# Kernel tuning notes

Hardware: AMD Instinct MI355X
Metric: run time of the kernel (lower is better)

Reference implementation:

```python
import jax, jax.numpy as jnp
import numpy as np

N_NODES = 100000
N_EDGES = 1600000
IN_CH = 128
OUT_CH = 64
HID = 2 * OUT_CH


def setup_inputs() -> dict:
    key = jax.random.key(0)
    ks = jax.random.split(key, 9)
    x = jax.random.normal(ks[0], (N_NODES, IN_CH), dtype=jnp.float32)
    edge_index = jax.random.randint(ks[1], (2, N_EDGES), 0, N_NODES, dtype=jnp.int64)
    s = 0.05
    W1 = jax.random.normal(ks[2], (IN_CH, HID), dtype=jnp.float32) * s
    b1 = jnp.zeros((HID,), dtype=jnp.float32)
    Wmu = jax.random.normal(ks[3], (HID, OUT_CH), dtype=jnp.float32) * s
    bmu = jnp.zeros((OUT_CH,), dtype=jnp.float32)
    Wls = jax.random.normal(ks[4], (HID, OUT_CH), dtype=jnp.float32) * s
    bls = jnp.zeros((OUT_CH,), dtype=jnp.float32)
    eps = jax.random.normal(ks[5], (N_NODES, OUT_CH), dtype=jnp.float32)
    return {"x": x, "edge_index": edge_index, "W1": W1, "b1": b1,
            "Wmu": Wmu, "bmu": bmu, "Wls": Wls, "bls": bls, "eps": eps}


def _gcn_conv(x, W, b, src, dst, dis):
    # PyG GCNConv: out = D^{-1/2}(A+I)D^{-1/2} X W + b, self-loops added.
    h = x @ W  # [N, F]
    norm = dis[src] * dis[dst]  # per-edge symmetric norm
    msg = h[src] * norm[:, None]  # [E, F] gathered + scaled messages
    agg = jax.ops.segment_sum(msg, dst, num_segments=x.shape[0])
    agg = agg + h * (dis * dis)[:, None]  # self-loop term
    return agg + b


def reference(x, edge_index, W1, b1, Wmu, bmu, Wls, bls, eps):
    src, dst = edge_index[0], edge_index[1]
    N = x.shape[0]
    # degree over A + I (aggregation at dst, +1 for self loop)
    deg = jax.ops.segment_sum(jnp.ones_like(dst, dtype=x.dtype), dst,
                              num_segments=N) + 1.0
    dis = jax.lax.rsqrt(deg)  # deg >= 1, safe
    h = _gcn_conv(x, W1, b1, src, dst, dis)
    mu = _gcn_conv(h, Wmu, bmu, src, dst, dis)
    logstd = _gcn_conv(h, Wls, bls, src, dst, dis)
    z = mu + eps * jnp.exp(logstd)  # reparametrization trick
    return (z, mu, logstd)
```

## Files before the change

kernel.cpp:

```cpp
#include <hip/hip_runtime.h>
#include <hip/hip_bf16.h>


typedef unsigned int u32;
typedef unsigned short u16;
typedef unsigned char u8;
typedef __bf16 bf16x8 __attribute__((ext_vector_type(8)));
typedef float f32x4 __attribute__((ext_vector_type(4)));
typedef int i32x4 __attribute__((ext_vector_type(4)));

__device__ __forceinline__ u16 f2bf(float f) {
    union { float f; u32 u; } v; v.f = f;
    u32 u = v.u;
    u += 0x7fffu + ((u >> 16) & 1u);
    return (u16)(u >> 16);
}
__device__ __forceinline__ float bflo(u32 p) {
    union { u32 u; float f; } v; v.u = p << 16; return v.f;
}
__device__ __forceinline__ float bfhi(u32 p) {
    union { u32 u; float f; } v; v.u = p & 0xffff0000u; return v.f;
}

__global__ __launch_bounds__(256) void deg_hist(const int* __restrict__ dst,
                                                u32* __restrict__ deg,
                                                u8* __restrict__ loc, int E) {
    int i4 = (blockIdx.x * 256 + threadIdx.x) * 4;
    if (i4 + 3 < E) {
        i32x4 d4 = __builtin_nontemporal_load((const i32x4*)(dst + i4));
        u32 l0 = atomicAdd(&deg[d4.x], 1u) & 0xffu;
        u32 l1 = atomicAdd(&deg[d4.y], 1u) & 0xffu;
        u32 l2 = atomicAdd(&deg[d4.z], 1u) & 0xffu;
        u32 l3 = atomicAdd(&deg[d4.w], 1u) & 0xffu;
        u32 packed = l0 | (l1 << 8) | (l2 << 16) | (l3 << 24);
        __builtin_nontemporal_store(packed, (u32*)(loc + i4));
    } else {
        for (int i = i4; i < E; ++i) loc[i] = (u8)atomicAdd(&deg[dst[i]], 1u);
    }
}

__global__ __launch_bounds__(256) void scanA(const u32* __restrict__ deg,
                                             u32* __restrict__ blockSums, int N) {
    __shared__ u32 s[256];
    int t = threadIdx.x, i = blockIdx.x * 256 + t;
    s[t] = (i < N) ? deg[i] : 0u;
    for (int off = 128; off > 0; off >>= 1) {
        __syncthreads();
        if (t < off) s[t] += s[t + off];
    }
    if (t == 0) blockSums[blockIdx.x] = s[0];
}

__global__ __launch_bounds__(512) void scanB(const u32* __restrict__ blockSums,
                                             u32* __restrict__ blockOffs, int NB) {
    __shared__ u32 s[512];
    int t = threadIdx.x;
    u32 v = (t < NB) ? blockSums[t] : 0u;
    s[t] = v;
    for (int off = 1; off < 512; off <<= 1) {
        __syncthreads();
        u32 add = (t >= off) ? s[t - off] : 0u;
        __syncthreads();
        s[t] += add;
    }
    __syncthreads();
    if (t < NB) blockOffs[t] = s[t] - v;
}

__global__ __launch_bounds__(256) void scanC(const u32* __restrict__ deg,
                                             const u32* __restrict__ blockOffs,
                                             u32* __restrict__ rowstart,
                                             float* __restrict__ dis, int N, int E) {
    __shared__ u32 s[256];
    int t = threadIdx.x, i = blockIdx.x * 256 + t;
    u32 v = (i < N) ? deg[i] : 0u;
    s[t] = v;
    for (int off = 1; off < 256; off <<= 1) {
        __syncthreads();
        u32 add = (t >= off) ? s[t - off] : 0u;
        __syncthreads();
        s[t] += add;
    }
    __syncthreads();
    if (i < N) {
        rowstart[i] = blockOffs[blockIdx.x] + s[t] - v;
        dis[i] = rsqrtf((float)v + 1.0f);
    }
    if (i == 0) rowstart[N] = (u32)E;
}

__global__ __launch_bounds__(256) void place_kernel(const int* __restrict__ src,
                                                    const int* __restrict__ dst,
                                                    const u8* __restrict__ loc,
                                                    const u32* __restrict__ rowstart,
                                                    int* __restrict__ csr, int E) {
    int i4 = (blockIdx.x * 256 + threadIdx.x) * 4;
    if (i4 + 3 < E) {
        i32x4 s4 = __builtin_nontemporal_load((const i32x4*)(src + i4));
        i32x4 d4 = __builtin_nontemporal_load((const i32x4*)(dst + i4));
        u32 l4 = __builtin_nontemporal_load((const u32*)(loc + i4));
        csr[rowstart[d4.x] + (l4 & 0xffu)] = s4.x;
        csr[rowstart[d4.y] + ((l4 >> 8) & 0xffu)] = s4.y;
        csr[rowstart[d4.z] + ((l4 >> 16) & 0xffu)] = s4.z;
        csr[rowstart[d4.w] + (l4 >> 24)] = s4.w;
    } else {
        for (int i = i4; i < E; ++i) csr[rowstart[dst[i]] + loc[i]] = src[i];
    }
}

__global__ __launch_bounds__(256) void fuse_w(const float* __restrict__ W1,
                                              const float* __restrict__ Wmu,
                                              const float* __restrict__ Wls,
                                              const float* __restrict__ b1,
                                              const float* __restrict__ bmu,
                                              const float* __restrict__ bls,
                                              u16* __restrict__ WfT,
                                              float* __restrict__ bb,
                                              float* __restrict__ bcat) {
    int idx = blockIdx.x * 256 + threadIdx.x;
    if (idx >= 16384) return;
    int k = idx >> 7, n = idx & 127;
    const float* Wcol = (n < 64) ? (Wmu + n) : (Wls + (n - 64));
    float acc = 0.f;
#pragma unroll 8
    for (int j = 0; j < 128; ++j) acc += W1[k * 128 + j] * Wcol[j * 64];
    WfT[n * 128 + k] = f2bf(acc);
    if (k == 0) {
        float accb = 0.f;
#pragma unroll 8
        for (int j = 0; j < 128; ++j) accb += b1[j] * Wcol[j * 64];
        bb[n] = accb;
        bcat[n] = (n < 64) ? bmu[n] : bls[n - 64];
    }
}

__global__ __launch_bounds__(256) void convert_x(const float* __restrict__ x,
                                                 const float* __restrict__ dis,
                                                 u32* __restrict__ xs,
                                                 u32* __restrict__ ts, int N) {
    long i = (long)blockIdx.x * 256 + threadIdx.x;
    long node = i >> 5;
    if (node > N) return;
    if (node == N) {
        ((uint2*)xs)[i] = make_uint2(0u, 0u);
        ((uint2*)ts)[i] = make_uint2(0u, 0u);
        return;
    }
    float dd = dis[node];
    f32x4 v = ((const f32x4*)x)[i];
    u32 p0 = (u32)f2bf(v[0] * dd) | ((u32)f2bf(v[1] * dd) << 16);
    u32 p1 = (u32)f2bf(v[2] * dd) | ((u32)f2bf(v[3] * dd) << 16);
    ((uint2*)xs)[i] = make_uint2(p0, p1);
}

__global__ __launch_bounds__(512) void g1gemm(const u32* __restrict__ xs,
                                              const int* __restrict__ csr,
                                              const u32* __restrict__ rowstart,
                                              const float* __restrict__ dis,
                                              const u16* __restrict__ WfT,
                                              const float* __restrict__ bb,
                                              u16* __restrict__ ts, int N) {
    __shared__ __align__(16) u16 ytile[16][136];
    __shared__ float disS[16];
    int tid = threadIdx.x, blk = blockIdx.x;
    int wave = tid >> 6, lane = tid & 63;
    int nsub = lane >> 5;
    int h = (lane >> 4) & 1;
    int l = lane & 15;
    int nl = wave * 2 + nsub;
    int node = blk * 16 + nl;
    bool live = node < N;
    int nodeC = live ? node : 0;
    float dd = dis[nodeC];
    u32 beg = live ? rowstart[nodeC] : 0u;
    u32 end = live ? rowstart[nodeC + 1] : 0u;
    u32 cut = beg + ((end - beg + 1u) >> 1);
    u32 mybeg = h ? cut : beg;
    u32 myend = h ? end : cut;
    if (tid < 16) disS[tid] = (blk * 16 + tid < N) ? dis[blk * 16 + tid] : 0.f;

    const uint4* xs4 = (const uint4*)xs;
    uint4 selfv = xs4[(long)nodeC * 16 + l];
    bool h0 = (h == 0);
    float a0 = h0 ? bflo(selfv.x) : 0.f, a1 = h0 ? bfhi(selfv.x) : 0.f;
    float a2 = h0 ? bflo(selfv.y) : 0.f, a3 = h0 ? bfhi(selfv.y) : 0.f;
    float a4 = h0 ? bflo(selfv.z) : 0.f, a5 = h0 ? bfhi(selfv.z) : 0.f;
    float a6 = h0 ? bflo(selfv.w) : 0.f, a7 = h0 ? bfhi(selfv.w) : 0.f;

    int sbase = nsub * 32 + h * 16;
    int s = (l < 8 && mybeg + (u32)l < myend) ? csr[mybeg + l] : N;
    for (u32 e0 = mybeg; e0 < myend; e0 += 8) {
        u32 e1 = e0 + 8;
        int sn = (l < 8 && e1 < myend && e1 + (u32)l < myend) ? csr[e1 + l] : N;
        uint4 w[8];
#pragma unroll
        for (int j = 0; j < 8; ++j) {
            int sj = __shfl(s, sbase + j);
            w[j] = xs4[(long)sj * 16 + l];
        }
#pragma unroll
        for (int j = 0; j < 8; ++j) {
            a0 += bflo(w[j].x); a1 += bfhi(w[j].x);
            a2 += bflo(w[j].y); a3 += bfhi(w[j].y);
            a4 += bflo(w[j].z); a5 += bfhi(w[j].z);
            a6 += bflo(w[j].w); a7 += bfhi(w[j].w);
        }
        s = sn;
    }
    a0 += __shfl_xor(a0, 16); a1 += __shfl_xor(a1, 16);
    a2 += __shfl_xor(a2, 16); a3 += __shfl_xor(a3, 16);
    a4 += __shfl_xor(a4, 16); a5 += __shfl_xor(a5, 16);
    a6 += __shfl_xor(a6, 16); a7 += __shfl_xor(a7, 16);

    uint4 o = make_uint4(0u, 0u, 0u, 0u);
    if (live) {
        o.x = (u32)f2bf(a0 * dd) | ((u32)f2bf(a1 * dd) << 16);
        o.y = (u32)f2bf(a2 * dd) | ((u32)f2bf(a3 * dd) << 16);
        o.z = (u32)f2bf(a4 * dd) | ((u32)f2bf(a5 * dd) << 16);
        o.w = (u32)f2bf(a6 * dd) | ((u32)f2bf(a7 * dd) << 16);
    }
    if (h0) *(uint4*)&ytile[nl][l * 8] = o;
    __syncthreads();

    int quad = lane >> 4, mn = l;
    bf16x8 af[4];
#pragma unroll
    for (int kk = 0; kk < 4; ++kk)
        af[kk] = *reinterpret_cast<const bf16x8*>(&ytile[mn][kk * 32 + quad * 8]);

    int col = wave * 16 + mn;
    f32x4 acc = {0.f, 0.f, 0.f, 0.f};
#pragma unroll
    for (int kk = 0; kk < 4; ++kk) {
        bf16x8 bf =
            *reinterpret_cast<const bf16x8*>(&WfT[col * 128 + kk * 32 + quad * 8]);
        acc = __builtin_amdgcn_mfma_f32_16x16x32_bf16(af[kk], bf, acc, 0, 0, 0);
    }
    float bc = bb[col];
#pragma unroll
    for (int r = 0; r < 4; ++r) {
        int row = quad * 4 + r;
        int gn = blk * 16 + row;
        if (gn < N)
            __builtin_nontemporal_store(f2bf((acc[r] + bc) * disS[row]),
                                        ts + (long)gn * 128 + col);
    }
}

__global__ __launch_bounds__(256) void gather2(const u32* __restrict__ ts,
                                               const int* __restrict__ csr,
                                               const u32* __restrict__ rowstart,
                                               const float* __restrict__ dis,
                                               const float* __restrict__ bcat,
                                               const float* __restrict__ eps,
                                               float* __restrict__ out, int N) {
    int tid = threadIdx.x;
    int gw = (blockIdx.x * 256 + tid) >> 6;
    int lane = tid & 63;
    int nsub = lane >> 5, h = (lane >> 4) & 1, l = lane & 15;
    int node = gw * 2 + nsub;
    bool live = node < N;
    int nodeC = live ? node : 0;
    float dd = dis[nodeC];
    u32 beg = live ? rowstart[nodeC] : 0u;
    u32 end = live ? rowstart[nodeC + 1] : 0u;
    u32 cut = beg + ((end - beg + 1u) >> 1);
    u32 mybeg = h ? cut : beg;
    u32 myend = h ? end : cut;
    const uint4* ts4 = (const uint4*)ts;

    uint4 selfv = ts4[(long)nodeC * 16 + l];
    bool h0 = (h == 0);
    float a0 = h0 ? bflo(selfv.x) : 0.f, a1 = h0 ? bfhi(selfv.x) : 0.f;
    float a2 = h0 ? bflo(selfv.y) : 0.f, a3 = h0 ? bfhi(selfv.y) : 0.f;
    float a4 = h0 ? bflo(selfv.z) : 0.f, a5 = h0 ? bfhi(selfv.z) : 0.f;
    float a6 = h0 ? bflo(selfv.w) : 0.f, a7 = h0 ? bfhi(selfv.w) : 0.f;

    int sbase = nsub * 32 + h * 16;
    int s = (l < 8 && mybeg + (u32)l < myend) ? csr[mybeg + l] : N;
    for (u32 e0 = mybeg; e0 < myend; e0 += 8) {
        u32 e1 = e0 + 8;
        int sn = (l < 8 && e1 < myend && e1 + (u32)l < myend) ? csr[e1 + l] : N;
        uint4 w[8];
#pragma unroll
        for (int j = 0; j < 8; ++j) {
            int sj = __shfl(s, sbase + j);
            w[j] = ts4[(long)sj * 16 + l];
        }
#pragma unroll
        for (int j = 0; j < 8; ++j) {
            a0 += bflo(w[j].x); a1 += bfhi(w[j].x);
            a2 += bflo(w[j].y); a3 += bfhi(w[j].y);
            a4 += bflo(w[j].z); a5 += bfhi(w[j].z);
            a6 += bflo(w[j].w); a7 += bfhi(w[j].w);
        }
        s = sn;
    }
    a0 += __shfl_xor(a0, 16); a1 += __shfl_xor(a1, 16);
    a2 += __shfl_xor(a2, 16); a3 += __shfl_xor(a3, 16);
    a4 += __shfl_xor(a4, 16); a5 += __shfl_xor(a5, 16);
    a6 += __shfl_xor(a6, 16); a7 += __shfl_xor(a7, 16);

    int c0 = l * 8;
    f32x4 clo = ((const f32x4*)bcat)[2 * l], chi = ((const f32x4*)bcat)[2 * l + 1];
    float v0 = a0 * dd + clo[0];
    float v1 = a1 * dd + clo[1];
    float v2 = a2 * dd + clo[2];
    float v3 = a3 * dd + clo[3];
    float v4 = a4 * dd + chi[0];
    float v5 = a5 * dd + chi[1];
    float v6 = a6 * dd + chi[2];
    float v7 = a7 * dd + chi[3];

    int srcl = lane + 8;
    float w0 = __shfl(v0, srcl), w1 = __shfl(v1, srcl), w2 = __shfl(v2, srcl),
          w3 = __shfl(v3, srcl), w4 = __shfl(v4, srcl), w5 = __shfl(v5, srcl),
          w6 = __shfl(v6, srcl), w7 = __shfl(v7, srcl);

    if (!live || h != 0) return;
    long NO = (long)N * 64;
    if (l < 8) {
        float* mu = out + NO + (long)node * 64 + c0;
        __builtin_nontemporal_store(f32x4{v0, v1, v2, v3}, (f32x4*)mu);
        __builtin_nontemporal_store(f32x4{v4, v5, v6, v7}, (f32x4*)mu + 1);
        const f32x4* ep = (const f32x4*)(eps + (long)node * 64 + c0);
        f32x4 e0v = __builtin_nontemporal_load(ep);
        f32x4 e1v = __builtin_nontemporal_load(ep + 1);
        float* z = out + (long)node * 64 + c0;
        f32x4 z0 = {v0 + e0v[0] * __expf(w0), v1 + e0v[1] * __expf(w1),
                    v2 + e0v[2] * __expf(w2), v3 + e0v[3] * __expf(w3)};
        f32x4 z1 = {v4 + e1v[0] * __expf(w4), v5 + e1v[1] * __expf(w5),
                    v6 + e1v[2] * __expf(w6), v7 + e1v[3] * __expf(w7)};
        __builtin_nontemporal_store(z0, (f32x4*)z);
        __builtin_nontemporal_store(z1, (f32x4*)z + 1);
    } else {
        float* ls = out + 2 * NO + (long)node * 64 + (c0 - 64);
        __builtin_nontemporal_store(f32x4{v0, v1, v2, v3}, (f32x4*)ls);
        __builtin_nontemporal_store(f32x4{v4, v5, v6, v7}, (f32x4*)ls + 1);
    }
}

extern "C" void kernel_launch(void* const* d_in, const int* in_sizes, int n_in,
                              void* d_out, int out_size, void* d_ws, size_t ws_size,
                              hipStream_t stream) {
    const float* x   = (const float*)d_in[0];
    const int* ei    = (const int*)d_in[1];
    const float* W1  = (const float*)d_in[2];
    const float* b1  = (const float*)d_in[3];
    const float* Wmu = (const float*)d_in[4];
    const float* bmu = (const float*)d_in[5];
    const float* Wls = (const float*)d_in[6];
    const float* bls = (const float*)d_in[7];
    const float* eps = (const float*)d_in[8];
    float* out = (float*)d_out;

    const int N = in_sizes[0] / 128;
    const int E = in_sizes[1] / 2;
    const int* src = ei;
    const int* dst = ei + E;
    const int NB = (N + 255) / 256;

    char* ws = (char*)d_ws;
    u32* deg       = (u32*)(ws + 0);
    u32* rowstart  = (u32*)(ws + 401408);
    u32* blockSums = (u32*)(ws + 802816);
    u32* blockOffs = (u32*)(ws + 804864);
    float* dis     = (float*)(ws + 806912);
    u16* WfT       = (u16*)(ws + 1208320);
    float* bb      = (float*)(ws + 1241088);
    float* bcat    = (float*)(ws + 1241600);
    u8* loc        = (u8*)(ws + 1242112);
    int* csr       = (int*)(ws + 2842112);
    u32* xs        = (u32*)(ws + 9242112);
    u32* ts        = (u32*)(ws + 34842368);

    hipMemsetAsync(deg, 0, 400000, stream);

    int gridE4 = (E / 4 + 255) / 256;
    deg_hist<<<gridE4, 256, 0, stream>>>(dst, deg, loc, E);
    scanA<<<NB, 256, 0, stream>>>(deg, blockSums, N);
    scanB<<<1, 512, 0, stream>>>(blockSums, blockOffs, NB);
    scanC<<<NB, 256, 0, stream>>>(deg, blockOffs, rowstart, dis, N, E);
    place_kernel<<<gridE4, 256, 0, stream>>>(src, dst, loc, rowstart, csr, E);
    fuse_w<<<64, 256, 0, stream>>>(W1, Wmu, Wls, b1, bmu, bls, WfT, bb, bcat);

    long Qc = (long)(N + 1) * 32;
    convert_x<<<(int)((Qc + 255) / 256), 256, 0, stream>>>(x, dis, xs, ts, N);

    int gridT = (N + 15) / 16;
    g1gemm<<<gridT, 512, 0, stream>>>(xs, csr, rowstart, dis, WfT, bb,
                                      (u16*)ts, N);

    int gridG = (((N + 1) / 2 + 3) / 4);
    gather2<<<gridG, 256, 0, stream>>>(ts, csr, rowstart, dis, bcat, eps, out, N);
}
```

Baseline: 411.3 us.

## Process nodes in degree-sorted order to balance gather work across waves

```diff
diff --git a/kernel.cpp b/kernel.cpp
--- a/kernel.cpp
+++ b/kernel.cpp
@@ -106,6 +106,48 @@
     } else {
         for (int i = i4; i < E; ++i) csr[rowstart[dst[i]] + loc[i]] = src[i];
     }
+}
+
+__global__ __launch_bounds__(256) void sortA(const u32* __restrict__ deg,
+                                             u32* __restrict__ bins, int N) {
+    __shared__ u32 h[256];
+    int t = threadIdx.x, i = blockIdx.x * 256 + t;
+    h[t] = 0;
+    __syncthreads();
+    if (i < N) atomicAdd(&h[deg[i] & 255u], 1u);
+    __syncthreads();
+    if (h[t]) atomicAdd(&bins[t], h[t]);
+}
+
+__global__ __launch_bounds__(256) void sortB(const u32* __restrict__ bins,
+                                             u32* __restrict__ binStart) {
+    __shared__ u32 s[256];
+    int t = threadIdx.x;
+    u32 v = bins[t];
+    s[t] = v;
+    for (int off = 1; off < 256; off <<= 1) {
+        __syncthreads();
+        u32 add = (t >= off) ? s[t - off] : 0u;
+        __syncthreads();
+        s[t] += add;
+    }
+    __syncthreads();
+    binStart[t] = s[t] - v;
+}
+
+__global__ __launch_bounds__(256) void sortC(const u32* __restrict__ deg,
+                                             u32* __restrict__ binCur,
+                                             u32* __restrict__ perm, int N) {
+    __shared__ u32 h[256], base[256];
+    int t = threadIdx.x, i = blockIdx.x * 256 + t;
+    h[t] = 0;
+    __syncthreads();
+    u32 d = 0, lh = 0;
+    if (i < N) { d = deg[i] & 255u; lh = atomicAdd(&h[d], 1u); }
+    __syncthreads();
+    if (h[t]) base[t] = atomicAdd(&binCur[t], h[t]);
+    __syncthreads();
+    if (i < N) perm[base[d] + lh] = (u32)i;
 }
 
 __global__ __launch_bounds__(256) void fuse_w(const float* __restrict__ W1,
@@ -157,30 +199,37 @@
                                               const int* __restrict__ csr,
                                               const u32* __restrict__ rowstart,
                                               const float* __restrict__ dis,
+                                              const u32* __restrict__ perm,
                                               const u16* __restrict__ WfT,
                                               const float* __restrict__ bb,
                                               u16* __restrict__ ts, int N) {
     __shared__ __align__(16) u16 ytile[16][136];
     __shared__ float disS[16];
+    __shared__ u32 permS[16];
     int tid = threadIdx.x, blk = blockIdx.x;
     int wave = tid >> 6, lane = tid & 63;
     int nsub = lane >> 5;
     int h = (lane >> 4) & 1;
     int l = lane & 15;
     int nl = wave * 2 + nsub;
-    int node = blk * 16 + nl;
-    bool live = node < N;
-    int nodeC = live ? node : 0;
-    float dd = dis[nodeC];
-    u32 beg = live ? rowstart[nodeC] : 0u;
-    u32 end = live ? rowstart[nodeC + 1] : 0u;
+    int slot = blk * 16 + nl;
+    bool live = slot < N;
+    int node = live ? (int)perm[slot] : 0;
+    float dd = dis[node];
+    u32 beg = live ? rowstart[node] : 0u;
+    u32 end = live ? rowstart[node + 1] : 0u;
     u32 cut = beg + ((end - beg + 1u) >> 1);
     u32 mybeg = h ? cut : beg;
     u32 myend = h ? end : cut;
-    if (tid < 16) disS[tid] = (blk * 16 + tid < N) ? dis[blk * 16 + tid] : 0.f;
+    if (tid < 16) {
+        int s2 = blk * 16 + tid;
+        u32 pn = (s2 < N) ? perm[s2] : 0u;
+        permS[tid] = pn;
+        disS[tid] = (s2 < N) ? dis[pn] : 0.f;
+    }
 
     const uint4* xs4 = (const uint4*)xs;
-    uint4 selfv = xs4[(long)nodeC * 16 + l];
+    uint4 selfv = xs4[(long)node * 16 + l];
     bool h0 = (h == 0);
     float a0 = h0 ? bflo(selfv.x) : 0.f, a1 = h0 ? bfhi(selfv.x) : 0.f;
     float a2 = h0 ? bflo(selfv.y) : 0.f, a3 = h0 ? bfhi(selfv.y) : 0.f;
@@ -240,10 +289,9 @@
 #pragma unroll
     for (int r = 0; r < 4; ++r) {
         int row = quad * 4 + r;
-        int gn = blk * 16 + row;
-        if (gn < N)
+        if (blk * 16 + row < N)
             __builtin_nontemporal_store(f2bf((acc[r] + bc) * disS[row]),
-                                        ts + (long)gn * 128 + col);
+                                        ts + (long)permS[row] * 128 + col);
     }
 }
 
@@ -251,6 +299,7 @@
                                                const int* __restrict__ csr,
                                                const u32* __restrict__ rowstart,
                                                const float* __restrict__ dis,
+                                               const u32* __restrict__ perm,
                                                const float* __restrict__ bcat,
                                                const float* __restrict__ eps,
                                                float* __restrict__ out, int N) {
@@ -258,18 +307,18 @@
     int gw = (blockIdx.x * 256 + tid) >> 6;
     int lane = tid & 63;
     int nsub = lane >> 5, h = (lane >> 4) & 1, l = lane & 15;
-    int node = gw * 2 + nsub;
-    bool live = node < N;
-    int nodeC = live ? node : 0;
-    float dd = dis[nodeC];
-    u32 beg = live ? rowstart[nodeC] : 0u;
-    u32 end = live ? rowstart[nodeC + 1] : 0u;
+    int slot = gw * 2 + nsub;
+    bool live = slot < N;
+    int node = live ? (int)perm[slot] : 0;
+    float dd = dis[node];
+    u32 beg = live ? rowstart[node] : 0u;
+    u32 end = live ? rowstart[node + 1] : 0u;
     u32 cut = beg + ((end - beg + 1u) >> 1);
     u32 mybeg = h ? cut : beg;
     u32 myend = h ? end : cut;
     const uint4* ts4 = (const uint4*)ts;
 
-    uint4 selfv = ts4[(long)nodeC * 16 + l];
+    uint4 selfv = ts4[(long)node * 16 + l];
     bool h0 = (h == 0);
     float a0 = h0 ? bflo(selfv.x) : 0.f, a1 = h0 ? bfhi(selfv.x) : 0.f;
     float a2 = h0 ? bflo(selfv.y) : 0.f, a3 = h0 ? bfhi(selfv.y) : 0.f;
@@ -373,6 +422,7 @@
     int* csr       = (int*)(ws + 2842112);
     u32* xs        = (u32*)(ws + 9242112);
     u32* ts        = (u32*)(ws + 34842368);
+    u32* perm      = (u32*)loc;
 
     hipMemsetAsync(deg, 0, 400000, stream);
 
@@ -382,15 +432,22 @@
     scanB<<<1, 512, 0, stream>>>(blockSums, blockOffs, NB);
     scanC<<<NB, 256, 0, stream>>>(deg, blockOffs, rowstart, dis, N, E);
     place_kernel<<<gridE4, 256, 0, stream>>>(src, dst, loc, rowstart, csr, E);
+
+    hipMemsetAsync(blockSums, 0, 1024, stream);
+    sortA<<<NB, 256, 0, stream>>>(deg, blockSums, N);
+    sortB<<<1, 256, 0, stream>>>(blockSums, blockOffs);
+    sortC<<<NB, 256, 0, stream>>>(deg, blockOffs, perm, N);
+
     fuse_w<<<64, 256, 0, stream>>>(W1, Wmu, Wls, b1, bmu, bls, WfT, bb, bcat);
 
     long Qc = (long)(N + 1) * 32;
     convert_x<<<(int)((Qc + 255) / 256), 256, 0, stream>>>(x, dis, xs, ts, N);
 
     int gridT = (N + 15) / 16;
-    g1gemm<<<gridT, 512, 0, stream>>>(xs, csr, rowstart, dis, WfT, bb,
+    g1gemm<<<gridT, 512, 0, stream>>>(xs, csr, rowstart, dis, perm, WfT, bb,
                                       (u16*)ts, N);
 
-    int gridG = (((N + 1) / 2 + 3) / 4);
-    gather2<<<gridG, 256, 0, stream>>>(ts, csr, rowstart, dis, bcat, eps, out, N);
-}
+    int gridG = (N + 7) / 8;
+    gather2<<<gridG, 256, 0, stream>>>(ts, csr, rowstart, dis, perm, bcat, eps,
+                                       out, N);
+}
```

New measurement: 430.9 us. +4.8%, slower.

## Build CSR via two-level bucket sort with shared-memory atomics

Applied to the files above, without the earlier changes.

```diff
diff --git a/kernel.cpp b/kernel.cpp
--- a/kernel.cpp
+++ b/kernel.cpp
@@ -9,6 +9,9 @@
 typedef float f32x4 __attribute__((ext_vector_type(4)));
 typedef int i32x4 __attribute__((ext_vector_type(4)));
 
+#define NBKT 196
+#define BSH 9
+
 __device__ __forceinline__ u16 f2bf(float f) {
     union { float f; u32 u; } v; v.f = f;
     u32 u = v.u;
@@ -22,58 +25,35 @@
     union { u32 u; float f; } v; v.u = p & 0xffff0000u; return v.f;
 }
 
-__global__ __launch_bounds__(256) void deg_hist(const int* __restrict__ dst,
-                                                u32* __restrict__ deg,
-                                                u8* __restrict__ loc, int E) {
-    int i4 = (blockIdx.x * 256 + threadIdx.x) * 4;
-    if (i4 + 3 < E) {
-        i32x4 d4 = __builtin_nontemporal_load((const i32x4*)(dst + i4));
-        u32 l0 = atomicAdd(&deg[d4.x], 1u) & 0xffu;
-        u32 l1 = atomicAdd(&deg[d4.y], 1u) & 0xffu;
-        u32 l2 = atomicAdd(&deg[d4.z], 1u) & 0xffu;
-        u32 l3 = atomicAdd(&deg[d4.w], 1u) & 0xffu;
-        u32 packed = l0 | (l1 << 8) | (l2 << 16) | (l3 << 24);
-        __builtin_nontemporal_store(packed, (u32*)(loc + i4));
+__global__ __launch_bounds__(256) void bcount(const int* __restrict__ dst,
+                                              u32* __restrict__ bucketCnt, int E) {
+    __shared__ u32 hist[NBKT];
+    int t = threadIdx.x;
+    for (int i = t; i < NBKT; i += 256) hist[i] = 0;
+    __syncthreads();
+    int base = (blockIdx.x * 256 + t) * 4;
+    if (base + 3 < E) {
+        i32x4 d4 = __builtin_nontemporal_load((const i32x4*)(dst + base));
+        atomicAdd(&hist[d4.x >> BSH], 1u);
+        atomicAdd(&hist[d4.y >> BSH], 1u);
+        atomicAdd(&hist[d4.z >> BSH], 1u);
+        atomicAdd(&hist[d4.w >> BSH], 1u);
     } else {
-        for (int i = i4; i < E; ++i) loc[i] = (u8)atomicAdd(&deg[dst[i]], 1u);
-    }
-}
-
-__global__ __launch_bounds__(256) void scanA(const u32* __restrict__ deg,
-                                             u32* __restrict__ blockSums, int N) {
+        for (int i = base; i < E; ++i) atomicAdd(&hist[dst[i] >> BSH], 1u);
+    }
+    __syncthreads();
+    for (int i = t; i < NBKT; i += 256)
+        if (hist[i]) atomicAdd(&bucketCnt[i], hist[i]);
+}
+
+__global__ __launch_bounds__(256) void bscan(const u32* __restrict__ bucketCnt,
+                                             u32* __restrict__ bucketStart,
+                                             u32* __restrict__ bucketCur,
+                                             u32* __restrict__ rowstart,
+                                             int N, int E) {
     __shared__ u32 s[256];
-    int t = threadIdx.x, i = blockIdx.x * 256 + t;
-    s[t] = (i < N) ? deg[i] : 0u;
-    for (int off = 128; off > 0; off >>= 1) {
-        __syncthreads();
-        if (t < off) s[t] += s[t + off];
-    }
-    if (t == 0) blockSums[blockIdx.x] = s[0];
-}
-
-__global__ __launch_bounds__(512) void scanB(const u32* __restrict__ blockSums,
-                                             u32* __restrict__ blockOffs, int NB) {
-    __shared__ u32 s[512];
     int t = threadIdx.x;
-    u32 v = (t < NB) ? blockSums[t] : 0u;
-    s[t] = v;
-    for (int off = 1; off < 512; off <<= 1) {
-        __syncthreads();
-        u32 add = (t >= off) ? s[t - off] : 0u;
-        __syncthreads();
-        s[t] += add;
-    }
-    __syncthreads();
-    if (t < NB) blockOffs[t] = s[t] - v;
-}
-
-__global__ __launch_bounds__(256) void scanC(const u32* __restrict__ deg,
-                                             const u32* __restrict__ blockOffs,
-                                             u32* __restrict__ rowstart,
-                                             float* __restrict__ dis, int N, int E) {
-    __shared__ u32 s[256];
-    int t = threadIdx.x, i = blockIdx.x * 256 + t;
-    u32 v = (i < N) ? deg[i] : 0u;
+    u32 v = (t < NBKT) ? bucketCnt[t] : 0u;
     s[t] = v;
     for (int off = 1; off < 256; off <<= 1) {
         __syncthreads();
@@ -82,29 +62,118 @@
         s[t] += add;
     }
     __syncthreads();
-    if (i < N) {
-        rowstart[i] = blockOffs[blockIdx.x] + s[t] - v;
-        dis[i] = rsqrtf((float)v + 1.0f);
-    }
-    if (i == 0) rowstart[N] = (u32)E;
-}
-
-__global__ __launch_bounds__(256) void place_kernel(const int* __restrict__ src,
-                                                    const int* __restrict__ dst,
-                                                    const u8* __restrict__ loc,
-                                                    const u32* __restrict__ rowstart,
-                                                    int* __restrict__ csr, int E) {
-    int i4 = (blockIdx.x * 256 + threadIdx.x) * 4;
-    if (i4 + 3 < E) {
-        i32x4 s4 = __builtin_nontemporal_load((const i32x4*)(src + i4));
-        i32x4 d4 = __builtin_nontemporal_load((const i32x4*)(dst + i4));
-        u32 l4 = __builtin_nontemporal_load((const u32*)(loc + i4));
-        csr[rowstart[d4.x] + (l4 & 0xffu)] = s4.x;
-        csr[rowstart[d4.y] + ((l4 >> 8) & 0xffu)] = s4.y;
-        csr[rowstart[d4.z] + ((l4 >> 16) & 0xffu)] = s4.z;
-        csr[rowstart[d4.w] + (l4 >> 24)] = s4.w;
+    if (t < NBKT) {
+        u32 ex = s[t] - v;
+        bucketStart[t] = ex;
+        bucketCur[t] = ex;
+        if (t == NBKT - 1) bucketStart[NBKT] = s[t];
+    }
+    if (t == 0) rowstart[N] = (u32)E;
+}
+
+__global__ __launch_bounds__(256) void bscatter(const int* __restrict__ src,
+                                                const int* __restrict__ dst,
+                                                u32* __restrict__ bucketCur,
+                                                u32* __restrict__ bksrc,
+                                                u32* __restrict__ bkdst, int E) {
+    __shared__ u32 hist[NBKT], lstart[NBKT], gbase[NBKT];
+    __shared__ u32 sA[256];
+    __shared__ u32 stS[1024], stD[1024];
+    int t = threadIdx.x;
+    int e0 = blockIdx.x * 1024;
+    int m = min(1024, E - e0);
+    for (int i = t; i < NBKT; i += 256) hist[i] = 0;
+    __syncthreads();
+
+    int sv[4], dv[4]; u32 rk[4];
+    int base = e0 + t * 4;
+    bool vec = (base + 3 < E);
+    if (vec) {
+        i32x4 s4 = __builtin_nontemporal_load((const i32x4*)(src + base));
+        i32x4 d4 = __builtin_nontemporal_load((const i32x4*)(dst + base));
+        sv[0] = s4.x; sv[1] = s4.y; sv[2] = s4.z; sv[3] = s4.w;
+        dv[0] = d4.x; dv[1] = d4.y; dv[2] = d4.z; dv[3] = d4.w;
+#pragma unroll
+        for (int j = 0; j < 4; ++j) rk[j] = atomicAdd(&hist[dv[j] >> BSH], 1u);
     } else {
-        for (int i = i4; i < E; ++i) csr[rowstart[dst[i]] + loc[i]] = src[i];
+#pragma unroll
+        for (int j = 0; j < 4; ++j) {
+            if (base + j < E) {
+                sv[j] = src[base + j]; dv[j] = dst[base + j];
+                rk[j] = atomicAdd(&hist[dv[j] >> BSH], 1u);
+            }
+        }
+    }
+    __syncthreads();
+    sA[t] = (t < NBKT) ? hist[t] : 0u;
+    for (int off = 1; off < 256; off <<= 1) {
+        __syncthreads();
+        u32 add = (t >= off) ? sA[t - off] : 0u;
+        __syncthreads();
+        sA[t] += add;
+    }
+    __syncthreads();
+    if (t < NBKT) {
+        lstart[t] = sA[t] - hist[t];
+        if (hist[t]) gbase[t] = atomicAdd(&bucketCur[t], hist[t]);
+    }
+    __syncthreads();
+#pragma unroll
+    for (int j = 0; j < 4; ++j) {
+        if (base + j < E) {
+            int b = dv[j] >> BSH;
+            u32 p = lstart[b] + rk[j];
+            stS[p] = (u32)sv[j];
+            stD[p] = (u32)dv[j];
+        }
+    }
+    __syncthreads();
+    for (int i = t; i < m; i += 256) {
+        u32 d = stD[i];
+        int b = (int)(d >> BSH);
+        u32 g = gbase[b] + ((u32)i - lstart[b]);
+        bksrc[g] = stS[i];
+        bkdst[g] = d;
+    }
+}
+
+__global__ __launch_bounds__(512) void bbuild(const u32* __restrict__ bksrc,
+                                              const u32* __restrict__ bkdst,
+                                              const u32* __restrict__ bucketStart,
+                                              u32* __restrict__ rowstart,
+                                              float* __restrict__ dis,
+                                              int* __restrict__ csr, int N) {
+    __shared__ u32 degL[512], exL[512];
+    int t = threadIdx.x, b = blockIdx.x;
+    int n0 = b << BSH;
+    int nn = min(N - n0, 512);
+    u32 ebeg = bucketStart[b], eend = bucketStart[b + 1];
+    degL[t] = 0;
+    __syncthreads();
+    for (u32 e = ebeg + t; e < eend; e += 512)
+        atomicAdd(&degL[bkdst[e] - (u32)n0], 1u);
+    __syncthreads();
+    u32 v = degL[t];
+    exL[t] = v;
+    for (int off = 1; off < 512; off <<= 1) {
+        __syncthreads();
+        u32 add = (t >= off) ? exL[t - off] : 0u;
+        __syncthreads();
+        exL[t] += add;
+    }
+    __syncthreads();
+    u32 absbase = ebeg + exL[t] - v;
+    if (t < nn) {
+        rowstart[n0 + t] = absbase;
+        dis[n0 + t] = rsqrtf((float)v + 1.0f);
+    }
+    __syncthreads();
+    exL[t] = absbase;
+    __syncthreads();
+    for (u32 e = ebeg + t; e < eend; e += 512) {
+        u32 ln = bkdst[e] - (u32)n0;
+        u32 pos = atomicAdd(&exL[ln], 1u);
+        csr[pos] = (int)bksrc[e];
     }
 }
 
@@ -358,30 +427,31 @@
     const int E = in_sizes[1] / 2;
     const int* src = ei;
     const int* dst = ei + E;
-    const int NB = (N + 255) / 256;
 
     char* ws = (char*)d_ws;
-    u32* deg       = (u32*)(ws + 0);
-    u32* rowstart  = (u32*)(ws + 401408);
-    u32* blockSums = (u32*)(ws + 802816);
-    u32* blockOffs = (u32*)(ws + 804864);
-    float* dis     = (float*)(ws + 806912);
-    u16* WfT       = (u16*)(ws + 1208320);
-    float* bb      = (float*)(ws + 1241088);
-    float* bcat    = (float*)(ws + 1241600);
-    u8* loc        = (u8*)(ws + 1242112);
-    int* csr       = (int*)(ws + 2842112);
-    u32* xs        = (u32*)(ws + 9242112);
-    u32* ts        = (u32*)(ws + 34842368);
-
-    hipMemsetAsync(deg, 0, 400000, stream);
+    u32* rowstart   = (u32*)(ws + 401408);
+    u32* bucketCnt  = (u32*)(ws + 802816);
+    u32* bucketStart= (u32*)(ws + 804864);
+    float* dis      = (float*)(ws + 806912);
+    u16* WfT        = (u16*)(ws + 1208320);
+    float* bb       = (float*)(ws + 1241088);
+    float* bcat     = (float*)(ws + 1241600);
+    u32* bucketCur  = (u32*)(ws + 1242112);
+    int* csr        = (int*)(ws + 2842112);
+    u32* xs         = (u32*)(ws + 9242112);
+    u32* ts         = (u32*)(ws + 34842368);
+    u32* bksrc      = (u32*)(ws + 34842368);
+    u32* bkdst      = (u32*)(ws + 41242368);
+
+    hipMemsetAsync(bucketCnt, 0, 1024, stream);
 
     int gridE4 = (E / 4 + 255) / 256;
-    deg_hist<<<gridE4, 256, 0, stream>>>(dst, deg, loc, E);
-    scanA<<<NB, 256, 0, stream>>>(deg, blockSums, N);
-    scanB<<<1, 512, 0, stream>>>(blockSums, blockOffs, NB);
-    scanC<<<NB, 256, 0, stream>>>(deg, blockOffs, rowstart, dis, N, E);
-    place_kernel<<<gridE4, 256, 0, stream>>>(src, dst, loc, rowstart, csr, E);
+    bcount<<<gridE4, 256, 0, stream>>>(dst, bucketCnt, E);
+    bscan<<<1, 256, 0, stream>>>(bucketCnt, bucketStart, bucketCur, rowstart, N, E);
+    bscatter<<<gridE4, 256, 0, stream>>>(src, dst, bucketCur, bksrc, bkdst, E);
+    bbuild<<<NBKT, 512, 0, stream>>>(bksrc, bkdst, bucketStart, rowstart, dis,
+                                     csr, N);
+
     fuse_w<<<64, 256, 0, stream>>>(W1, Wmu, Wls, b1, bmu, bls, WfT, bb, bcat);
 
     long Qc = (long)(N + 1) * 32;
```

Result: faster. 390.4 us (-5.1%).
